# Kernel optimization log

Measured on AMD Instinct MI355X. Metric: run time of the kernel, lower is better.

The kernel has to match this reference:

```python
import jax, jax.numpy as jnp
import numpy as np

N_HEADS = 16


def setup_inputs() -> dict:
    key = jax.random.key(0)
    ks = jax.random.split(key, 8)
    B, T, D = 2, 2048, 1024
    hd, rank = D // N_HEADS, 32
    std = 0.02
    inp = {
        "x": jax.random.normal(ks[0], (B, T, D), jnp.float32),
        "Wq": jax.random.normal(ks[1], (D, D), jnp.float32) * std,
        "bq": jnp.zeros((D,), jnp.float32),
        "Wk": jax.random.normal(ks[2], (D, D), jnp.float32) * std,
        "bk": jnp.zeros((D,), jnp.float32),
        "Wv": jax.random.normal(ks[3], (D, D), jnp.float32) * std,
        "bv": jnp.zeros((D,), jnp.float32),
        "Wo": jax.random.normal(ks[4], (D, D), jnp.float32) * std,
        "bo": jnp.zeros((D,), jnp.float32),
        # orthogonal-ish init via QR, matching nn.init.orthogonal_
        "U": jnp.linalg.qr(jax.random.normal(ks[5], (hd, rank), jnp.float32))[0],
        "V": jnp.linalg.qr(jax.random.normal(ks[6], (hd, rank), jnp.float32))[0],
    }
    return inp


def reference(x, Wq, bq, Wk, bk, Wv, bv, Wo, bo, U, V):
    B, T, D = x.shape
    H = N_HEADS
    hd = D // H
    rank = V.shape[1]
    # torch Linear: y = x @ W.T + b
    q = (x @ Wq.T + bq).reshape(B, T, H, hd).transpose(0, 2, 1, 3)  # [B,H,T,hd]
    k = (x @ Wk.T + bk).reshape(B, T, H, hd).transpose(0, 2, 1, 3)
    v = (x @ Wv.T + bv).reshape(B, T, H, hd).transpose(0, 2, 1, 3)
    # low-rank subspace projection (shared V across heads)
    zq = q @ V  # [B,H,T,rank]
    zk = k @ V
    zv = v @ V
    att = jnp.einsum("bhqr,bhkr->bhqk", zq, zk) / jnp.sqrt(jnp.float32(max(rank, 1)))
    att = jax.nn.softmax(att, axis=-1)
    y_r = jnp.einsum("bhqk,bhkr->bhqr", att, zv)  # [B,H,T,rank]
    y = y_r @ U.T  # reconstruct to [B,H,T,hd]
    y = y.transpose(0, 2, 1, 3).reshape(B, T, D)
    return y @ Wo.T + bo
```

## Files before the change

kernel.cpp:

```cpp
#include <hip/hip_runtime.h>
#include <hip/hip_bf16.h>
#include <cstdint>

#define NB 2
#define NT 2048
#define ND 1024
#define NH 16
#define HD 64
#define RANK 32
#define HR 512

typedef _Float16 f16;
typedef _Float16 f16x2 __attribute__((ext_vector_type(2)));
typedef _Float16 f16x4 __attribute__((ext_vector_type(4)));
typedef _Float16 f16x8 __attribute__((ext_vector_type(8)));
typedef float f32x4 __attribute__((ext_vector_type(4)));

#define ZQ_SCALE 0.2550696805f

__device__ __forceinline__ float fast_exp2(float x) {
#if __has_builtin(__builtin_amdgcn_exp2f)
  return __builtin_amdgcn_exp2f(x);
#else
  return exp2f(x);
#endif
}

__global__ __launch_bounds__(256) void conv_f16(const float* __restrict__ in,
                                                f16* __restrict__ out, int n8) {
  int i = blockIdx.x * 256 + threadIdx.x;
  if (i >= n8) return;
  const float4* p = (const float4*)in + (size_t)i * 2;
  float4 a = p[0], b = p[1];
  f16x8 h = {(f16)a.x, (f16)a.y, (f16)a.z, (f16)a.w,
             (f16)b.x, (f16)b.y, (f16)b.z, (f16)b.w};
  *(f16x8*)(out + (size_t)i * 8) = h;
}

__global__ __launch_bounds__(256) void prep_wp(
    const float* __restrict__ Wq, const float* __restrict__ Wk,
    const float* __restrict__ Wv, const float* __restrict__ V,
    f16* __restrict__ WqPT, f16* __restrict__ WkPT, f16* __restrict__ WvPT)
{
  __shared__ float Vs[HD][RANK];
  const int tid = threadIdx.x;
  const int Dp  = blockIdx.x * 256 + tid;
  const int h   = blockIdx.y;
  const int m   = blockIdx.z;
  const float* W = m == 0 ? Wq : m == 1 ? Wk : Wv;
  f16*         O = m == 0 ? WqPT : m == 1 ? WkPT : WvPT;
  const float scale = m == 0 ? ZQ_SCALE : 1.0f;

  for (int i = tid; i < HD * RANK; i += 256) Vs[i >> 5][i & 31] = V[i];
  __syncthreads();

  float acc[RANK] = {};
#pragma unroll 4
  for (int d = 0; d < HD; ++d) {
    float w = W[(size_t)(h * HD + d) * ND + Dp];
#pragma unroll
    for (int r = 0; r < RANK; ++r) acc[r] = fmaf(w, Vs[d][r], acc[r]);
  }
#pragma unroll
  for (int r = 0; r < RANK; ++r)
    O[(size_t)(h * RANK + r) * ND + Dp] = (f16)(acc[r] * scale);
}

__global__ __launch_bounds__(512) void prep_bp(
    const float* __restrict__ bq, const float* __restrict__ bk,
    const float* __restrict__ bv, const float* __restrict__ V,
    float* __restrict__ bqp, float* __restrict__ bkp, float* __restrict__ bvp)
{
  const int m  = blockIdx.x;
  const int hr = threadIdx.x;
  const float* bs = m == 0 ? bq : m == 1 ? bk : bv;
  float*       o  = m == 0 ? bqp : m == 1 ? bkp : bvp;
  const int h = hr >> 5, r = hr & 31;
  float a = 0.f;
#pragma unroll
  for (int d = 0; d < HD; ++d) a = fmaf(bs[h * HD + d], V[d * RANK + r], a);
  o[hr] = a * (m == 0 ? ZQ_SCALE : 1.0f);
}

#define GBM 128
#define GBN 64
#define GBK 64

__device__ __forceinline__ int swz(int b) { return b ^ (((b >> 7) & 7) << 4); }

__device__ __forceinline__ void gload16(const f16* g, const f16* lds_wave_base) {
  __builtin_amdgcn_global_load_lds(
      (const __attribute__((address_space(1))) void*)g,
      (__attribute__((address_space(3))) void*)lds_wave_base, 16, 0, 0);
}

template <typename OT, bool ROWBIAS>
__global__ __launch_bounds__(256) void gemm_f16_bias(
    const f16* __restrict__ A, const f16* __restrict__ W,
    const float* __restrict__ bias, OT* __restrict__ C, int M, int N, int K)
{
  __shared__ f16 sA[GBM * GBK];
  __shared__ f16 sB[GBN * GBK];
  const int tid  = threadIdx.x;
  const int wid  = tid >> 6;
  const int lane = tid & 63;
  const int bm = blockIdx.x * GBM;
  const int bn = blockIdx.y * GBN;
  const int wm = (wid >> 1) * 64;
  const int wn = (wid & 1) * 32;

  f32x4 acc[4][2];
#pragma unroll
  for (int i = 0; i < 4; ++i)
#pragma unroll
    for (int j = 0; j < 2; ++j) acc[i][j] = (f32x4){0.f, 0.f, 0.f, 0.f};

  int arow[4], aoff[4];
#pragma unroll
  for (int i = 0; i < 4; ++i) {
    int Lg = swz(i * 4096 + tid * 16);
    arow[i] = Lg >> 7;
    aoff[i] = (Lg & 127) >> 1;
  }
  int brow[2], boff[2];
#pragma unroll
  for (int i = 0; i < 2; ++i) {
    int Lg = swz(i * 4096 + tid * 16);
    brow[i] = Lg >> 7;
    boff[i] = (Lg & 127) >> 1;
  }

  const char* sAc = (const char*)sA;
  const char* sBc = (const char*)sB;

  for (int k0 = 0; k0 < K; k0 += GBK) {
    __syncthreads();
#pragma unroll
    for (int i = 0; i < 4; ++i)
      gload16(A + (size_t)(bm + arow[i]) * K + k0 + aoff[i],
              (const f16*)((const char*)sA + i * 4096 + wid * 1024));
#pragma unroll
    for (int i = 0; i < 2; ++i)
      gload16(W + (size_t)(bn + brow[i]) * K + k0 + boff[i],
              (const f16*)((const char*)sB + i * 4096 + wid * 1024));
    __syncthreads();

#pragma unroll
    for (int kh = 0; kh < 2; ++kh) {
      const int kb = kh * 64 + ((lane >> 4) << 4);
      f16x8 af[4], bf[2];
#pragma unroll
      for (int mi = 0; mi < 4; ++mi) {
        int Lg = (wm + mi * 16 + (lane & 15)) * 128 + kb;
        af[mi] = *(const f16x8*)(sAc + swz(Lg));
      }
#pragma unroll
      for (int ni = 0; ni < 2; ++ni) {
        int Lg = (wn + ni * 16 + (lane & 15)) * 128 + kb;
        bf[ni] = *(const f16x8*)(sBc + swz(Lg));
      }
#pragma unroll
      for (int mi = 0; mi < 4; ++mi)
#pragma unroll
        for (int ni = 0; ni < 2; ++ni)
          acc[mi][ni] = __builtin_amdgcn_mfma_f32_16x16x32_f16(
              af[mi], bf[ni], acc[mi][ni], 0, 0, 0);
    }
  }

  const int cl = lane & 15, rh = lane >> 4;
#pragma unroll
  for (int ni = 0; ni < 2; ++ni) {
    const int col = bn + wn + ni * 16 + cl;
    const float cb = ROWBIAS ? 0.f : bias[col];
#pragma unroll
    for (int mi = 0; mi < 4; ++mi) {
      const int r0 = bm + wm + mi * 16 + rh * 4;
#pragma unroll
      for (int r = 0; r < 4; ++r) {
        const float bb = ROWBIAS ? bias[r0 + r] : cb;
        C[(size_t)(r0 + r) * N + col] = (OT)(acc[mi][ni][r] + bb);
      }
    }
  }
}

#define QBLK 64
#define KBLK 64
#define SKLD 40

__global__ __launch_bounds__(256) void attn_mfma(
    const f16* __restrict__ zq,
    const f16* __restrict__ zk,
    const f16* __restrict__ zvT,
    float* __restrict__ y_r)
{
  __shared__ f16 sK[KBLK * SKLD];
  __shared__ f16 sVT[RANK * KBLK];
  __shared__ f16 sP[4][16 * KBLK];
  __shared__ float sL[4][16];

  const int tid  = threadIdx.x;
  const int wid  = tid >> 6;
  const int lane = tid & 63;
  const int g    = lane >> 4;
  const int m16  = lane & 15;
  const int bh   = blockIdx.y;
  const int b    = bh >> 4;
  const int h    = bh & 15;
  const int q0   = blockIdx.x * QBLK + wid * 16;

  const f16* zqb = zq + (size_t)b * NT * HR + h * RANK;
  const f16* zkb = zk + (size_t)b * NT * HR + h * RANK;
  const char* zvb = (const char*)zvT;

  f16x8 qfrag = *(const f16x8*)(zqb + (size_t)(q0 + m16) * HR + g * 8);

  const int zk_row = tid >> 2, zk_c = tid & 3;
  const int zv_r = tid >> 3;
  const int zv_srcoff = ((tid & 7) * 16) ^ ((zv_r & 7) << 4);
  const size_t zv_rowbase = ((size_t)(h * RANK + zv_r) * NB + b) * (NT * 2);

  f32x4 acc0 = {0.f, 0.f, 0.f, 0.f}, acc1 = {0.f, 0.f, 0.f, 0.f};
  float lpart = 0.f;

  char* sPw = (char*)&sP[wid][0];
  char* sVTc = (char*)sVT;
  const int swzq = (m16 & 7) << 4;

  for (int k0 = 0; k0 < NT; k0 += KBLK) {
    f16x8 kreg = *(const f16x8*)(zkb + (size_t)(k0 + zk_row) * HR + zk_c * 8);
    __syncthreads();
    __builtin_amdgcn_global_load_lds(
        (const __attribute__((address_space(1))) void*)(
            zvb + zv_rowbase + k0 * 2 + zv_srcoff),
        (__attribute__((address_space(3))) void*)(sVTc + wid * 1024), 16, 0, 0);
    *(f16x8*)(sK + zk_row * SKLD + zk_c * 8) = kreg;
    __syncthreads();

    f32x4 s[4];
#pragma unroll
    for (int kt = 0; kt < 4; ++kt) {
      f16x8 kf = *(const f16x8*)(sK + (kt * 16 + m16) * SKLD + g * 8);
      f32x4 z4 = {0.f, 0.f, 0.f, 0.f};
      s[kt] = __builtin_amdgcn_mfma_f32_16x16x32_f16(kf, qfrag, z4, 0, 0, 0);
    }

#pragma unroll
    for (int kt = 0; kt < 4; ++kt) {
      float p0 = fast_exp2(s[kt][0]);
      float p1 = fast_exp2(s[kt][1]);
      float p2 = fast_exp2(s[kt][2]);
      float p3 = fast_exp2(s[kt][3]);
      lpart += (p0 + p1) + (p2 + p3);
      f16x4 pk = {(f16)p0, (f16)p1, (f16)p2, (f16)p3};
      *(f16x4*)(sPw + m16 * 128 + ((kt * 32 + g * 8) ^ swzq)) = pk;
    }

#pragma unroll
    for (int kt2 = 0; kt2 < 2; ++kt2) {
      const int rb = kt2 * 64 + g * 16;
      f16x8 pf = *(const f16x8*)(sPw + m16 * 128 + (rb ^ swzq));
      f16x8 v0 = *(const f16x8*)(sVTc + m16 * 128 + (rb ^ swzq));
      f16x8 v1 = *(const f16x8*)(sVTc + (16 + m16) * 128 + (rb ^ swzq));
      acc0 = __builtin_amdgcn_mfma_f32_16x16x32_f16(pf, v0, acc0, 0, 0, 0);
      acc1 = __builtin_amdgcn_mfma_f32_16x16x32_f16(pf, v1, acc1, 0, 0, 0);
    }
  }

  lpart += __shfl_xor(lpart, 16);
  lpart += __shfl_xor(lpart, 32);
  if (lane < 16) sL[wid][lane] = lpart;
  __syncthreads();

  float* yb = y_r + ((size_t)bh * NT + q0) * RANK;
#pragma unroll
  for (int r = 0; r < 4; ++r) {
    const float inv = 1.f / sL[wid][g * 4 + r];
    yb[(size_t)(g * 4 + r) * RANK + m16]      = acc0[r] * inv;
    yb[(size_t)(g * 4 + r) * RANK + 16 + m16] = acc1[r] * inv;
  }
}

__global__ __launch_bounds__(256) void urecon(
    const float* __restrict__ y_r, const float* __restrict__ U,
    f16* __restrict__ y_h)
{
  __shared__ float Us[HD][RANK];
  const int tid = threadIdx.x;
  for (int i = tid; i < HD * RANK; i += 256) Us[i >> 5][i & 31] = U[i];
  __syncthreads();

  const int gi = blockIdx.x * 256 + tid;
  const int bh = gi >> 11;
  const int t  = gi & (NT - 1);
  const int b  = bh >> 4;
  const int h  = bh & 15;

  const float* yr = y_r + (size_t)gi * RANK;
  float a[RANK];
#pragma unroll
  for (int r4 = 0; r4 < 8; ++r4) {
    float4 v4 = *(const float4*)(yr + r4 * 4);
    a[r4 * 4 + 0] = v4.x; a[r4 * 4 + 1] = v4.y;
    a[r4 * 4 + 2] = v4.z; a[r4 * 4 + 3] = v4.w;
  }

  f16* yrow = y_h + ((size_t)(b * NT) + t) * ND + h * HD;
#pragma unroll
  for (int d8 = 0; d8 < 8; ++d8) {
    f16x8 hv;
#pragma unroll
    for (int j = 0; j < 8; ++j) {
      float o = 0.f;
#pragma unroll
      for (int r = 0; r < RANK; ++r) o = fmaf(a[r], Us[d8 * 8 + j][r], o);
      hv[j] = (f16)o;
    }
    *(f16x8*)(yrow + d8 * 8) = hv;
  }
}

extern "C" void kernel_launch(void* const* d_in, const int* in_sizes, int n_in,
                              void* d_out, int out_size, void* d_ws, size_t ws_size,
                              hipStream_t stream) {
  const float* x  = (const float*)d_in[0];
  const float* Wq = (const float*)d_in[1];
  const float* bq = (const float*)d_in[2];
  const float* Wk = (const float*)d_in[3];
  const float* bk = (const float*)d_in[4];
  const float* Wv = (const float*)d_in[5];
  const float* bv = (const float*)d_in[6];
  const float* Wo = (const float*)d_in[7];
  const float* bo = (const float*)d_in[8];
  const float* U  = (const float*)d_in[9];
  const float* V  = (const float*)d_in[10];
  float* out = (float*)d_out;

  float* ws = (float*)d_ws;
  f16*   x_h  = (f16*)(ws + 0);
  f16*   WoH  = (f16*)(ws + 2097152);
  f16*   WqPT = (f16*)(ws + 2621440);
  f16*   WkPT = (f16*)(ws + 2883584);
  f16*   WvPT = (f16*)(ws + 3145728);
  float* bqp  = ws + 3407872;
  float* bkp  = ws + 3408384;
  float* bvp  = ws + 3408896;
  f16*   zq   = (f16*)(ws + 3409408);
  f16*   zk   = (f16*)(ws + 4457984);
  f16*   zvT  = (f16*)(ws + 5506560);
  float* y_r  = ws + 6555136;
  f16*   y_h  = (f16*)(ws + 8652288);

  conv_f16<<<2048, 256, 0, stream>>>(x, x_h, 524288);
  conv_f16<<<512, 256, 0, stream>>>(Wo, WoH, 131072);

  prep_wp<<<dim3(4, 16, 3), 256, 0, stream>>>(Wq, Wk, Wv, V, WqPT, WkPT, WvPT);
  prep_bp<<<3, 512, 0, stream>>>(bq, bk, bv, V, bqp, bkp, bvp);

  gemm_f16_bias<f16, false><<<dim3(32, 8), 256, 0, stream>>>(
      x_h, WqPT, bqp, zq, NB * NT, HR, ND);
  gemm_f16_bias<f16, false><<<dim3(32, 8), 256, 0, stream>>>(
      x_h, WkPT, bkp, zk, NB * NT, HR, ND);
  gemm_f16_bias<f16, true><<<dim3(4, 64), 256, 0, stream>>>(
      WvPT, x_h, bvp, zvT, HR, NB * NT, ND);

  dim3 ga(NT / QBLK, NB * NH);
  attn_mfma<<<ga, 256, 0, stream>>>(zq, zk, zvT, y_r);

  urecon<<<256, 256, 0, stream>>>(y_r, U, y_h);

  gemm_f16_bias<float, false><<<dim3(32, 16), 256, 0, stream>>>(
      y_h, WoH, bo, out, NB * NT, ND, ND);
}
```

Baseline: 238.5 us.

## Fold U reconstruction into Wo and merge Q/K projection GEMMs

Precomputes Wo·U per head so the output GEMM consumes the rank-32 attention output directly (K=512 instead of 1024). This removes the urecon kernel and the fp32 y_r round trip, and attention now writes f16 output in [B,T,H*rank] layout. The Q and K projection GEMMs are merged into a single GEMM with a combined 1024-wide output. The cost is an extra prep kernel and f16 rounding of the attention output before the final GEMM.

```diff
diff --git a/kernel.cpp b/kernel.cpp
--- a/kernel.cpp
+++ b/kernel.cpp
@@ -9,6 +9,7 @@
 #define HD 64
 #define RANK 32
 #define HR 512
+#define ZSTR 1024
 
 typedef _Float16 f16;
 typedef _Float16 f16x2 __attribute__((ext_vector_type(2)));
@@ -40,7 +41,7 @@
 __global__ __launch_bounds__(256) void prep_wp(
     const float* __restrict__ Wq, const float* __restrict__ Wk,
     const float* __restrict__ Wv, const float* __restrict__ V,
-    f16* __restrict__ WqPT, f16* __restrict__ WkPT, f16* __restrict__ WvPT)
+    f16* __restrict__ Oq, f16* __restrict__ Ok, f16* __restrict__ Ov)
 {
   __shared__ float Vs[HD][RANK];
   const int tid = threadIdx.x;
@@ -48,7 +49,7 @@
   const int h   = blockIdx.y;
   const int m   = blockIdx.z;
   const float* W = m == 0 ? Wq : m == 1 ? Wk : Wv;
-  f16*         O = m == 0 ? WqPT : m == 1 ? WkPT : WvPT;
+  f16*         O = m == 0 ? Oq : m == 1 ? Ok : Ov;
   const float scale = m == 0 ? ZQ_SCALE : 1.0f;
 
   for (int i = tid; i < HD * RANK; i += 256) Vs[i >> 5][i & 31] = V[i];
@@ -80,6 +81,39 @@
 #pragma unroll
   for (int d = 0; d < HD; ++d) a = fmaf(bs[h * HD + d], V[d * RANK + r], a);
   o[hr] = a * (m == 0 ? ZQ_SCALE : 1.0f);
+}
+
+__global__ __launch_bounds__(256) void prep_wo(
+    const float* __restrict__ Wo, const float* __restrict__ U,
+    f16* __restrict__ WoPP)
+{
+  __shared__ float Ws[64][65];
+  __shared__ float Us[HD][RANK];
+  const int tid = threadIdx.x;
+  const int n0  = blockIdx.x * 64;
+  const int h   = blockIdx.y;
+
+  for (int i = tid; i < HD * RANK; i += 256) Us[i >> 5][i & 31] = U[i];
+#pragma unroll
+  for (int it = 0; it < 16; ++it) {
+    int idx = it * 256 + tid;
+    int i = idx >> 6, d = idx & 63;
+    Ws[i][d] = Wo[(size_t)(n0 + i) * ND + h * HD + d];
+  }
+  __syncthreads();
+
+  const int i  = tid >> 2;
+  const int r0 = (tid & 3) << 3;
+  float acc[8] = {};
+#pragma unroll 4
+  for (int d = 0; d < HD; ++d) {
+    float w = Ws[i][d];
+#pragma unroll
+    for (int j = 0; j < 8; ++j) acc[j] = fmaf(w, Us[d][r0 + j], acc[j]);
+  }
+  f16x8 o = {(f16)acc[0], (f16)acc[1], (f16)acc[2], (f16)acc[3],
+             (f16)acc[4], (f16)acc[5], (f16)acc[6], (f16)acc[7]};
+  *(f16x8*)(WoPP + (size_t)(n0 + i) * HR + h * RANK + r0) = o;
 }
 
 #define GBM 128
@@ -190,10 +224,9 @@
 #define SKLD 40
 
 __global__ __launch_bounds__(256) void attn_mfma(
-    const f16* __restrict__ zq,
-    const f16* __restrict__ zk,
+    const f16* __restrict__ zqk,
     const f16* __restrict__ zvT,
-    float* __restrict__ y_r)
+    f16* __restrict__ y_rh)
 {
   __shared__ f16 sK[KBLK * SKLD];
   __shared__ f16 sVT[RANK * KBLK];
@@ -210,11 +243,11 @@
   const int h    = bh & 15;
   const int q0   = blockIdx.x * QBLK + wid * 16;
 
-  const f16* zqb = zq + (size_t)b * NT * HR + h * RANK;
-  const f16* zkb = zk + (size_t)b * NT * HR + h * RANK;
+  const f16* zqb = zqk + (size_t)b * NT * ZSTR + h * RANK;
+  const f16* zkb = zqk + (size_t)b * NT * ZSTR + HR + h * RANK;
   const char* zvb = (const char*)zvT;
 
-  f16x8 qfrag = *(const f16x8*)(zqb + (size_t)(q0 + m16) * HR + g * 8);
+  f16x8 qfrag = *(const f16x8*)(zqb + (size_t)(q0 + m16) * ZSTR + g * 8);
 
   const int zk_row = tid >> 2, zk_c = tid & 3;
   const int zv_r = tid >> 3;
@@ -229,7 +262,7 @@
   const int swzq = (m16 & 7) << 4;
 
   for (int k0 = 0; k0 < NT; k0 += KBLK) {
-    f16x8 kreg = *(const f16x8*)(zkb + (size_t)(k0 + zk_row) * HR + zk_c * 8);
+    f16x8 kreg = *(const f16x8*)(zkb + (size_t)(k0 + zk_row) * ZSTR + zk_c * 8);
     __syncthreads();
     __builtin_amdgcn_global_load_lds(
         (const __attribute__((address_space(1))) void*)(
@@ -273,51 +306,12 @@
   if (lane < 16) sL[wid][lane] = lpart;
   __syncthreads();
 
-  float* yb = y_r + ((size_t)bh * NT + q0) * RANK;
+  f16* yb = y_rh + ((size_t)(b * NT) + q0) * HR + h * RANK;
 #pragma unroll
   for (int r = 0; r < 4; ++r) {
     const float inv = 1.f / sL[wid][g * 4 + r];
-    yb[(size_t)(g * 4 + r) * RANK + m16]      = acc0[r] * inv;
-    yb[(size_t)(g * 4 + r) * RANK + 16 + m16] = acc1[r] * inv;
-  }
-}
-
-__global__ __launch_bounds__(256) void urecon(
-    const float* __restrict__ y_r, const float* __restrict__ U,
-    f16* __restrict__ y_h)
-{
-  __shared__ float Us[HD][RANK];
-  const int tid = threadIdx.x;
-  for (int i = tid; i < HD * RANK; i += 256) Us[i >> 5][i & 31] = U[i];
-  __syncthreads();
-
-  const int gi = blockIdx.x * 256 + tid;
-  const int bh = gi >> 11;
-  const int t  = gi & (NT - 1);
-  const int b  = bh >> 4;
-  const int h  = bh & 15;
-
-  const float* yr = y_r + (size_t)gi * RANK;
-  float a[RANK];
-#pragma unroll
-  for (int r4 = 0; r4 < 8; ++r4) {
-    float4 v4 = *(const float4*)(yr + r4 * 4);
-    a[r4 * 4 + 0] = v4.x; a[r4 * 4 + 1] = v4.y;
-    a[r4 * 4 + 2] = v4.z; a[r4 * 4 + 3] = v4.w;
-  }
-
-  f16* yrow = y_h + ((size_t)(b * NT) + t) * ND + h * HD;
-#pragma unroll
-  for (int d8 = 0; d8 < 8; ++d8) {
-    f16x8 hv;
-#pragma unroll
-    for (int j = 0; j < 8; ++j) {
-      float o = 0.f;
-#pragma unroll
-      for (int r = 0; r < RANK; ++r) o = fmaf(a[r], Us[d8 * 8 + j][r], o);
-      hv[j] = (f16)o;
-    }
-    *(f16x8*)(yrow + d8 * 8) = hv;
+    yb[(size_t)(g * 4 + r) * HR + m16]      = (f16)(acc0[r] * inv);
+    yb[(size_t)(g * 4 + r) * HR + 16 + m16] = (f16)(acc1[r] * inv);
   }
 }
 
@@ -338,38 +332,31 @@
   float* out = (float*)d_out;
 
   float* ws = (float*)d_ws;
-  f16*   x_h  = (f16*)(ws + 0);
-  f16*   WoH  = (f16*)(ws + 2097152);
-  f16*   WqPT = (f16*)(ws + 2621440);
-  f16*   WkPT = (f16*)(ws + 2883584);
-  f16*   WvPT = (f16*)(ws + 3145728);
-  float* bqp  = ws + 3407872;
-  float* bkp  = ws + 3408384;
-  float* bvp  = ws + 3408896;
-  f16*   zq   = (f16*)(ws + 3409408);
-  f16*   zk   = (f16*)(ws + 4457984);
-  f16*   zvT  = (f16*)(ws + 5506560);
-  float* y_r  = ws + 6555136;
-  f16*   y_h  = (f16*)(ws + 8652288);
+  f16*   x_h   = (f16*)(ws + 0);
+  f16*   WqkPT = (f16*)(ws + 2097152);
+  f16*   WvPT  = (f16*)(ws + 2621440);
+  f16*   WoPP  = (f16*)(ws + 2883584);
+  float* bqkp  = ws + 3145728;
+  float* bvp   = ws + 3146752;
+  f16*   zqk   = (f16*)(ws + 3147264);
+  f16*   zvT   = (f16*)(ws + 5244416);
+  f16*   y_rh  = (f16*)(ws + 6292992);
 
   conv_f16<<<2048, 256, 0, stream>>>(x, x_h, 524288);
-  conv_f16<<<512, 256, 0, stream>>>(Wo, WoH, 131072);
-
-  prep_wp<<<dim3(4, 16, 3), 256, 0, stream>>>(Wq, Wk, Wv, V, WqPT, WkPT, WvPT);
-  prep_bp<<<3, 512, 0, stream>>>(bq, bk, bv, V, bqp, bkp, bvp);
-
-  gemm_f16_bias<f16, false><<<dim3(32, 8), 256, 0, stream>>>(
-      x_h, WqPT, bqp, zq, NB * NT, HR, ND);
-  gemm_f16_bias<f16, false><<<dim3(32, 8), 256, 0, stream>>>(
-      x_h, WkPT, bkp, zk, NB * NT, HR, ND);
+
+  prep_wp<<<dim3(4, 16, 3), 256, 0, stream>>>(
+      Wq, Wk, Wv, V, WqkPT, WqkPT + 512 * 1024, WvPT);
+  prep_bp<<<3, 512, 0, stream>>>(bq, bk, bv, V, bqkp, bqkp + 512, bvp);
+  prep_wo<<<dim3(16, 16), 256, 0, stream>>>(Wo, U, WoPP);
+
+  gemm_f16_bias<f16, false><<<dim3(32, 16), 256, 0, stream>>>(
+      x_h, WqkPT, bqkp, zqk, NB * NT, ZSTR, ND);
   gemm_f16_bias<f16, true><<<dim3(4, 64), 256, 0, stream>>>(
       WvPT, x_h, bvp, zvT, HR, NB * NT, ND);
 
   dim3 ga(NT / QBLK, NB * NH);
-  attn_mfma<<<ga, 256, 0, stream>>>(zq, zk, zvT, y_r);
-
-  urecon<<<256, 256, 0, stream>>>(y_r, U, y_h);
+  attn_mfma<<<ga, 256, 0, stream>>>(zqk, zvT, y_rh);
 
   gemm_f16_bias<float, false><<<dim3(32, 16), 256, 0, stream>>>(
-      y_h, WoH, bo, out, NB * NT, ND, ND);
-}
+      y_rh, WoPP, bo, out, NB * NT, ND, HR);
+}
```

After: 198.7 us. 1.2x faster.
